# Performance work log

Hardware: AMD Instinct MI355X
Metric: run time of the kernel (lower is better)

## Reference

```python
import jax, jax.numpy as jnp
import numpy as np

HEAD_DIM = 64
NUM_HEADS = 16
ROPE_BASE = 10000.0


def _rope_cos_sin(seq_len, head_dim, dtype):
    inv_freq = 1.0 / (ROPE_BASE ** (jnp.arange(0, head_dim, 2, dtype=jnp.float32) / head_dim))
    t = jnp.arange(seq_len, dtype=jnp.float32)
    freqs = jnp.outer(t, inv_freq)                      # [S, D/2]
    emb = jnp.concatenate([freqs, freqs], axis=-1)      # [S, D]
    return jnp.cos(emb).astype(dtype), jnp.sin(emb).astype(dtype)


def _rotate_half(x):
    x1, x2 = jnp.split(x, 2, axis=-1)
    return jnp.concatenate([-x2, x1], axis=-1)


def setup_inputs() -> dict:
    key = jax.random.key(0)
    ks = jax.random.split(key, 5)
    B, S, H = 2, 2048, 1024
    x = jax.random.normal(ks[0], (B, S, H), dtype=jnp.float32)
    attention_mask = jnp.ones((B, S), dtype=jnp.float32)
    scale = 0.02
    Wq = jax.random.normal(ks[1], (H, H), dtype=jnp.float32) * scale
    Wk = jax.random.normal(ks[2], (H, H), dtype=jnp.float32) * scale
    Wv = jax.random.normal(ks[3], (H, H), dtype=jnp.float32) * scale
    Wo = jax.random.normal(ks[4], (H, H), dtype=jnp.float32) * scale
    return {"x": x, "attention_mask": attention_mask, "Wq": Wq, "Wk": Wk, "Wv": Wv, "Wo": Wo}


def reference(x, attention_mask, Wq, Wk, Wv, Wo):
    B, S, H = x.shape
    nh, hd = NUM_HEADS, HEAD_DIM
    scale = hd ** -0.5

    # nn.Linear semantics: y = x @ W^T  (W is [out, in])
    q = jnp.einsum('bsh,oh->bso', x, Wq).reshape(B, S, nh, hd).transpose(0, 2, 1, 3)
    k = jnp.einsum('bsh,oh->bso', x, Wk).reshape(B, S, nh, hd).transpose(0, 2, 1, 3)
    v = jnp.einsum('bsh,oh->bso', x, Wv).reshape(B, S, nh, hd).transpose(0, 2, 1, 3)

    cos, sin = _rope_cos_sin(S, hd, x.dtype)            # [S, hd]
    cos = cos[None, None, :, :]
    sin = sin[None, None, :, :]
    q = q * cos + _rotate_half(q) * sin
    k = k * cos + _rotate_half(k) * sin

    attn = jnp.einsum('bhqd,bhkd->bhqk', q, k) * scale  # [B, nh, S, S]
    mask = (1.0 - attention_mask.astype(x.dtype))[:, None, None, :] * jnp.finfo(x.dtype).min
    attn = attn + mask
    attn = jax.nn.softmax(attn, axis=-1)
    out = jnp.einsum('bhqk,bhkd->bhqd', attn, v)        # [B, nh, S, hd]
    out = out.transpose(0, 2, 1, 3).reshape(B, S, nh * hd)
    return jnp.einsum('bso,ho->bsh', out, Wo)
```

## Files before the change

### kernel.cpp

```cpp
#include <hip/hip_runtime.h>
#include <math.h>

#define BB 2
#define SS 2048
#define HH 1024
#define NH 16
#define HD 64
#define MM (BB*SS)

typedef __attribute__((ext_vector_type(8))) _Float16 f16x8;
typedef __attribute__((ext_vector_type(4))) float f32x4;

__device__ __forceinline__ unsigned short f2h(float f) {
    union { _Float16 h; unsigned short u; } c;
    c.h = (_Float16)f;
    return c.u;
}

__device__ __forceinline__ void gld16(const void* g, void* s) {
    __builtin_amdgcn_global_load_lds(
        (const __attribute__((address_space(1))) void*)g,
        (__attribute__((address_space(3))) void*)s, 16, 0, 0);
}

__global__ __launch_bounds__(256) void prep(
    const float* __restrict__ x,
    const float* __restrict__ Wq, const float* __restrict__ Wk,
    const float* __restrict__ Wv, const float* __restrict__ Wo,
    unsigned short* __restrict__ xf, unsigned short* __restrict__ wf,
    float* __restrict__ ctab, float* __restrict__ stab)
{
    int gtid = blockIdx.x * 256 + threadIdx.x;
    if (gtid < SS * 32) {
        int s = gtid >> 5, i = gtid & 31;
        double invf = pow(10000.0, -(double)i / 32.0);
        double a = (double)s * invf;
        ctab[gtid] = (float)cos(a);
        stab[gtid] = (float)sin(a);
    }
    for (int it = gtid; it < 2097152; it += 524288) {
        float4 v; unsigned short* d; size_t off;
        if (it < 1048576) {
            off = (size_t)it * 4;
            v = *(const float4*)(x + off);
            d = xf;
        } else {
            off = (size_t)(it - 1048576) * 4;
            int row = (int)(off >> 10);
            const float* W = row < 1024 ? Wq : row < 2048 ? Wk : row < 3072 ? Wv : Wo;
            v = *(const float4*)(W + (((size_t)(row & 1023)) << 10) + (off & 1023));
            d = wf;
        }
        *(ushort4*)(d + off) = make_ushort4(f2h(v.x), f2h(v.y), f2h(v.z), f2h(v.w));
    }
}

template<int MODE>
__global__ __launch_bounds__(256, 3) void gemm3(
    const unsigned short* __restrict__ Axf,
    const unsigned short* __restrict__ Wf,
    const float* __restrict__ ctab, const float* __restrict__ stab,
    unsigned short* __restrict__ qo, unsigned short* __restrict__ ko,
    unsigned short* __restrict__ vo, float* __restrict__ fout)
{
    __shared__ __align__(16) short lsA[2][128*32];
    __shared__ __align__(16) short lsB[2][128*32];

    const int t = threadIdx.x;
    const int m0 = blockIdx.x * 128;
    const int brow0 = (MODE == 0 ? 0 : 3072) + blockIdx.y * 128;
    const int lane = t & 63, wv = t >> 6;
    const int wm = (wv >> 1) * 64, wn = (wv & 1) * 64;
    const int fr = lane & 15, fg = lane >> 4;

    const int srow = t >> 2, pc = t & 3;
    const int scx = (pc ^ ((srow >> 1) & 3)) * 8;
    const int lo  = srow * 32 + pc * 8;
    const size_t gA0 = (size_t)(m0 + srow) * HH + scx;
    const size_t gA1 = (size_t)(m0 + 64 + srow) * HH + scx;
    const size_t gB0 = (size_t)(brow0 + srow) * HH + scx;
    const size_t gB1 = (size_t)(brow0 + 64 + srow) * HH + scx;

    f32x4 acc[4][4] = {};

#define STAGE(sel, kk) do { \
        gld16(Axf + gA0 + (kk), &lsA[sel][lo]);            \
        gld16(Wf  + gB0 + (kk), &lsB[sel][lo]);            \
        gld16(Axf + gA1 + (kk), &lsA[sel][lo + 64*32]);    \
        gld16(Wf  + gB1 + (kk), &lsB[sel][lo + 64*32]);    \
    } while (0)

    STAGE(0, 0);
    __syncthreads();

    int cur = 0;
    for (int k0 = 0; k0 < HH; k0 += 32) {
        if (k0 + 32 < HH) STAGE(cur ^ 1, k0 + 32);

        f16x8 ah[4], bh[4];
        const int swz = (fg ^ ((fr >> 1) & 3)) * 8;
        #pragma unroll
        for (int mi = 0; mi < 4; ++mi)
            ah[mi] = *(const f16x8*)&lsA[cur][(wm + 16*mi + fr)*32 + swz];
        #pragma unroll
        for (int ni = 0; ni < 4; ++ni)
            bh[ni] = *(const f16x8*)&lsB[cur][(wn + 16*ni + fr)*32 + swz];

        __builtin_amdgcn_s_setprio(1);
        #pragma unroll
        for (int mi = 0; mi < 4; ++mi)
            #pragma unroll
            for (int ni = 0; ni < 4; ++ni)
                acc[mi][ni] = __builtin_amdgcn_mfma_f32_16x16x32_f16(ah[mi], bh[ni], acc[mi][ni], 0, 0, 0);
        __builtin_amdgcn_s_setprio(0);
        __syncthreads();
        cur ^= 1;
    }
#undef STAGE

    if (MODE == 0) {
        const int mat = brow0 >> 10;
        const int obase = (brow0 & 1023) + wn;
        const int h = obase >> 6;
        #pragma unroll
        for (int mi = 0; mi < 4; ++mi)
            #pragma unroll
            for (int rr = 0; rr < 4; ++rr) {
                int m = m0 + wm + 16*mi + 4*fg + rr;
                int b = m >> 11, s = m & (SS - 1);
                float v[4];
                #pragma unroll
                for (int ni = 0; ni < 4; ++ni) v[ni] = acc[mi][ni][rr];
                if (mat < 2) {
                    #pragma unroll
                    for (int ni = 0; ni < 2; ++ni) {
                        int i = 16*ni + fr;
                        float c = ctab[s*32 + i], sn = stab[s*32 + i];
                        float v1 = v[ni], v2 = v[ni + 2];
                        v[ni]     = v1*c - v2*sn;
                        v[ni + 2] = v2*c + v1*sn;
                    }
                }
                size_t base = ((size_t)(b*NH + h) * SS + s) * HD;
                #pragma unroll
                for (int ni = 0; ni < 4; ++ni) {
                    int d = 16*ni + fr;
                    unsigned short hb = f2h(v[ni]);
                    if (mat == 0)      qo[base + d] = hb;
                    else if (mat == 1) ko[base + (d ^ ((s & 7) << 3))] = hb;
                    else {
                        size_t va = ((size_t)(b*NH + h) * HD + d) * SS
                                  + (s & ~63) + ((s & 63) ^ ((d & 7) << 3));
                        vo[va] = hb;
                    }
                }
            }
    } else {
        const int n0 = blockIdx.y * 128 + wn;
        #pragma unroll
        for (int mi = 0; mi < 4; ++mi)
            #pragma unroll
            for (int rr = 0; rr < 4; ++rr) {
                int m = m0 + wm + 16*mi + 4*fg + rr;
                #pragma unroll
                for (int ni = 0; ni < 4; ++ni)
                    fout[(size_t)m * HH + n0 + 16*ni + fr] = acc[mi][ni][rr];
            }
    }
}

__global__ __launch_bounds__(256, 4) void attn(
    const unsigned short* __restrict__ qg, const unsigned short* __restrict__ kg,
    const unsigned short* __restrict__ vtg, const float* __restrict__ mask,
    unsigned short* __restrict__ cf)
{
    __shared__ __align__(16) short Ks[2][64*64];
    __shared__ __align__(16) short Vs[2][64*64];
    __shared__ __align__(16) short Ps[64*64];

    const int t = threadIdx.x, lane = t & 63, wv = t >> 6;
    const int fr = lane & 15, fg = lane >> 4;
    const int bh = blockIdx.y, b = bh >> 4, h = bh & 15;
    const int q0 = blockIdx.x * 64;

    const unsigned short* kgb = kg  + (size_t)bh*SS*HD;
    const unsigned short* vgb = vtg + (size_t)bh*HD*SS;

    f16x8 qa[2];
    #pragma unroll
    for (int kc = 0; kc < 2; ++kc)
        qa[kc] = *(const f16x8*)&qg[((size_t)bh*SS + q0 + 16*wv + fr)*HD + kc*32 + fg*8];

    f32x4 o[4] = {};
    float lpart[4] = {0.f, 0.f, 0.f, 0.f};

    const int srow = t >> 3, sg = t & 7;

    gld16(kgb + (size_t)(srow)*HD + sg*8,      &Ks[0][srow*64 + sg*8]);
    gld16(kgb + (size_t)(32+srow)*HD + sg*8,   &Ks[0][(32+srow)*64 + sg*8]);
    gld16(vgb + (size_t)srow*SS + sg*8,        &Vs[0][srow*64 + sg*8]);
    gld16(vgb + (size_t)(32+srow)*SS + sg*8,   &Vs[0][(32+srow)*64 + sg*8]);
    __syncthreads();

    int cur = 0;
    for (int kt = 0; kt < SS/64; ++kt) {
        const int k0 = kt * 64;
        if (kt + 1 < SS/64) {
            const int kn = k0 + 64;
            gld16(kgb + (size_t)(kn+srow)*HD + sg*8,      &Ks[cur^1][srow*64 + sg*8]);
            gld16(kgb + (size_t)(kn+32+srow)*HD + sg*8,   &Ks[cur^1][(32+srow)*64 + sg*8]);
            gld16(vgb + (size_t)srow*SS + kn + sg*8,      &Vs[cur^1][srow*64 + sg*8]);
            gld16(vgb + (size_t)(32+srow)*SS + kn + sg*8, &Vs[cur^1][(32+srow)*64 + sg*8]);
        }

        f32x4 sc[4] = {};
        __builtin_amdgcn_s_setprio(1);
        #pragma unroll
        for (int kc = 0; kc < 2; ++kc) {
            f16x8 kb[4];
            #pragma unroll
            for (int nf = 0; nf < 4; ++nf) {
                int row = 16*nf + fr;
                int gr = (4*kc + fg) ^ (fr & 7);
                kb[nf] = *(const f16x8*)&Ks[cur][row*64 + gr*8];
            }
            #pragma unroll
            for (int nf = 0; nf < 4; ++nf)
                sc[nf] = __builtin_amdgcn_mfma_f32_16x16x32_f16(qa[kc], kb[nf], sc[nf], 0, 0, 0);
        }
        __builtin_amdgcn_s_setprio(0);

        float madd[4];
        #pragma unroll
        for (int nf = 0; nf < 4; ++nf)
            madd[nf] = (1.0f - mask[(size_t)b*SS + k0 + 16*nf + fr]) * (-1.0e38f);

        #pragma unroll
        for (int rr = 0; rr < 4; ++rr) {
            const int prow = 16*wv + 4*fg + rr;
            #pragma unroll
            for (int nf = 0; nf < 4; ++nf) {
                float p = __builtin_amdgcn_exp2f(fmaf(sc[nf][rr], 0.18033688f, madd[nf]));
                lpart[rr] += p;
                int col = 16*nf + fr;
                int gr = (col >> 3) ^ (prow & 7);
                Ps[prow*64 + gr*8 + (col & 7)] = (short)f2h(p);
            }
        }

        __builtin_amdgcn_s_setprio(1);
        #pragma unroll
        for (int kc = 0; kc < 2; ++kc) {
            int grk = (4*kc + fg) ^ (fr & 7);
            f16x8 pa = *(const f16x8*)&Ps[(16*wv + fr)*64 + grk*8];
            #pragma unroll
            for (int df = 0; df < 4; ++df) {
                f16x8 vb = *(const f16x8*)&Vs[cur][(16*df + fr)*64 + grk*8];
                o[df] = __builtin_amdgcn_mfma_f32_16x16x32_f16(pa, vb, o[df], 0, 0, 0);
            }
        }
        __builtin_amdgcn_s_setprio(0);
        __syncthreads();
        cur ^= 1;
    }

    #pragma unroll
    for (int rr = 0; rr < 4; ++rr) {
        float l = lpart[rr];
        #pragma unroll
        for (int d = 1; d < 16; d <<= 1) l += __shfl_xor(l, d);
        float inv = 1.0f / l;
        int srw = q0 + 16*wv + 4*fg + rr;
        size_t base = ((size_t)b*SS + srw)*HH + h*HD;
        #pragma unroll
        for (int df = 0; df < 4; ++df)
            cf[base + 16*df + fr] = f2h(o[df][rr] * inv);
    }
}

extern "C" void kernel_launch(void* const* d_in, const int* in_sizes, int n_in,
                              void* d_out, int out_size, void* d_ws, size_t ws_size,
                              hipStream_t stream) {
    const float* x    = (const float*)d_in[0];
    const float* mask = (const float*)d_in[1];
    const float* Wq   = (const float*)d_in[2];
    const float* Wk   = (const float*)d_in[3];
    const float* Wv   = (const float*)d_in[4];
    const float* Wo   = (const float*)d_in[5];
    float* out = (float*)d_out;

    const size_t T = (size_t)MM * HH;
    unsigned short* xf = (unsigned short*)d_ws;
    unsigned short* wf = xf + T;
    unsigned short* qt = wf + T;
    unsigned short* kt = qt + T;
    unsigned short* vt = kt + T;
    float* ctab = (float*)(vt + T);
    float* stab = ctab + SS*32;
    unsigned short* cf = xf;

    prep<<<2048, 256, 0, stream>>>(x, Wq, Wk, Wv, Wo, xf, wf, ctab, stab);
    gemm3<0><<<dim3(MM/128, 3*HH/128), 256, 0, stream>>>(xf, wf, ctab, stab,
                                                         qt, kt, vt, nullptr);
    attn<<<dim3(SS/64, BB*NH), 256, 0, stream>>>(qt, kt, vt, mask, cf);
    gemm3<1><<<dim3(MM/128, HH/128), 256, 0, stream>>>(cf, wf, nullptr, nullptr,
                                                       nullptr, nullptr, nullptr, out);
}
```

Baseline: 129.1 us.

## Enlarge attention tile to 128 queries, transpose MFMA operands, precompute mask and q scale

The attention kernel now runs 512 threads covering 128 query rows per block, so each K/V tile loaded into LDS serves twice as many queries and each thread issues only one load per tile. The MFMA operands are swapped so each lane holds four consecutive key scores for a single query row. That allows packed half-precision P stores, one running sum per lane, and packed vectorised output stores. The softmax scale is folded into Q in the projection GEMM, and the additive mask is precomputed once in prep and read as float4. Costs are fewer blocks (lower occupancy and less grid parallelism) and rounding of the pre-scaled Q to fp16.

```diff
diff --git a/kernel.cpp b/kernel.cpp
--- a/kernel.cpp
+++ b/kernel.cpp
@@ -9,7 +9,10 @@
 #define MM (BB*SS)
 
 typedef __attribute__((ext_vector_type(8))) _Float16 f16x8;
+typedef __attribute__((ext_vector_type(2))) __fp16 hf16x2;
 typedef __attribute__((ext_vector_type(4))) float f32x4;
+
+#define QSCALE 0.18033688011112042f
 
 __device__ __forceinline__ unsigned short f2h(float f) {
     union { _Float16 h; unsigned short u; } c;
@@ -17,6 +20,12 @@
     return c.u;
 }
 
+__device__ __forceinline__ unsigned int pkh(float a, float b) {
+    union { hf16x2 h; unsigned int u; } c;
+    c.h = __builtin_amdgcn_cvt_pkrtz(a, b);
+    return c.u;
+}
+
 __device__ __forceinline__ void gld16(const void* g, void* s) {
     __builtin_amdgcn_global_load_lds(
         (const __attribute__((address_space(1))) void*)g,
@@ -24,11 +33,11 @@
 }
 
 __global__ __launch_bounds__(256) void prep(
-    const float* __restrict__ x,
+    const float* __restrict__ x, const float* __restrict__ mask,
     const float* __restrict__ Wq, const float* __restrict__ Wk,
     const float* __restrict__ Wv, const float* __restrict__ Wo,
     unsigned short* __restrict__ xf, unsigned short* __restrict__ wf,
-    float* __restrict__ ctab, float* __restrict__ stab)
+    float* __restrict__ ctab, float* __restrict__ stab, float* __restrict__ mt)
 {
     int gtid = blockIdx.x * 256 + threadIdx.x;
     if (gtid < SS * 32) {
@@ -38,6 +47,8 @@
         ctab[gtid] = (float)cos(a);
         stab[gtid] = (float)sin(a);
     }
+    if (gtid < BB * SS)
+        mt[gtid] = (1.0f - mask[gtid]) * (-1.0e38f);
     for (int it = gtid; it < 2097152; it += 524288) {
         float4 v; unsigned short* d; size_t off;
         if (it < 1048576) {
@@ -140,6 +151,10 @@
                         v[ni]     = v1*c - v2*sn;
                         v[ni + 2] = v2*c + v1*sn;
                     }
+                }
+                if (mat == 0) {
+                    #pragma unroll
+                    for (int ni = 0; ni < 4; ++ni) v[ni] *= QSCALE;
                 }
                 size_t base = ((size_t)(b*NH + h) * SS + s) * HD;
                 #pragma unroll
@@ -169,22 +184,23 @@
     }
 }
 
-__global__ __launch_bounds__(256, 4) void attn(
+__global__ __launch_bounds__(512, 2) void attn(
     const unsigned short* __restrict__ qg, const unsigned short* __restrict__ kg,
-    const unsigned short* __restrict__ vtg, const float* __restrict__ mask,
+    const unsigned short* __restrict__ vtg, const float* __restrict__ mt,
     unsigned short* __restrict__ cf)
 {
     __shared__ __align__(16) short Ks[2][64*64];
     __shared__ __align__(16) short Vs[2][64*64];
-    __shared__ __align__(16) short Ps[64*64];
+    __shared__ __align__(16) short Ps[128*64];
 
     const int t = threadIdx.x, lane = t & 63, wv = t >> 6;
-    const int fr = lane & 15, fg = lane >> 4;
+    const int fr = lane & 15, fg = lane >> 4, frx = fr & 7;
     const int bh = blockIdx.y, b = bh >> 4, h = bh & 15;
-    const int q0 = blockIdx.x * 64;
+    const int q0 = blockIdx.x * 128;
 
     const unsigned short* kgb = kg  + (size_t)bh*SS*HD;
     const unsigned short* vgb = vtg + (size_t)bh*HD*SS;
+    const float* mtb = mt + (size_t)b*SS;
 
     f16x8 qa[2];
     #pragma unroll
@@ -192,14 +208,13 @@
         qa[kc] = *(const f16x8*)&qg[((size_t)bh*SS + q0 + 16*wv + fr)*HD + kc*32 + fg*8];
 
     f32x4 o[4] = {};
-    float lpart[4] = {0.f, 0.f, 0.f, 0.f};
+    float lpart = 0.f;
+    const int pbase = (wv*16 + fr) * 64;
 
     const int srow = t >> 3, sg = t & 7;
 
-    gld16(kgb + (size_t)(srow)*HD + sg*8,      &Ks[0][srow*64 + sg*8]);
-    gld16(kgb + (size_t)(32+srow)*HD + sg*8,   &Ks[0][(32+srow)*64 + sg*8]);
-    gld16(vgb + (size_t)srow*SS + sg*8,        &Vs[0][srow*64 + sg*8]);
-    gld16(vgb + (size_t)(32+srow)*SS + sg*8,   &Vs[0][(32+srow)*64 + sg*8]);
+    gld16(kgb + (size_t)srow*HD + sg*8, &Ks[0][srow*64 + sg*8]);
+    gld16(vgb + (size_t)srow*SS + sg*8, &Vs[0][srow*64 + sg*8]);
     __syncthreads();
 
     int cur = 0;
@@ -207,56 +222,48 @@
         const int k0 = kt * 64;
         if (kt + 1 < SS/64) {
             const int kn = k0 + 64;
-            gld16(kgb + (size_t)(kn+srow)*HD + sg*8,      &Ks[cur^1][srow*64 + sg*8]);
-            gld16(kgb + (size_t)(kn+32+srow)*HD + sg*8,   &Ks[cur^1][(32+srow)*64 + sg*8]);
-            gld16(vgb + (size_t)srow*SS + kn + sg*8,      &Vs[cur^1][srow*64 + sg*8]);
-            gld16(vgb + (size_t)(32+srow)*SS + kn + sg*8, &Vs[cur^1][(32+srow)*64 + sg*8]);
-        }
+            gld16(kgb + (size_t)(kn+srow)*HD + sg*8, &Ks[cur^1][srow*64 + sg*8]);
+            gld16(vgb + (size_t)srow*SS + kn + sg*8, &Vs[cur^1][srow*64 + sg*8]);
+        }
+
+        float4 m4[4];
+        #pragma unroll
+        for (int nf = 0; nf < 4; ++nf)
+            m4[nf] = *(const float4*)&mtb[k0 + 16*nf + 4*fg];
 
         f32x4 sc[4] = {};
         __builtin_amdgcn_s_setprio(1);
         #pragma unroll
         for (int kc = 0; kc < 2; ++kc) {
-            f16x8 kb[4];
             #pragma unroll
             for (int nf = 0; nf < 4; ++nf) {
-                int row = 16*nf + fr;
-                int gr = (4*kc + fg) ^ (fr & 7);
-                kb[nf] = *(const f16x8*)&Ks[cur][row*64 + gr*8];
+                int gr = (4*kc + fg) ^ frx;
+                f16x8 kb = *(const f16x8*)&Ks[cur][(16*nf + fr)*64 + gr*8];
+                sc[nf] = __builtin_amdgcn_mfma_f32_16x16x32_f16(kb, qa[kc], sc[nf], 0, 0, 0);
             }
-            #pragma unroll
-            for (int nf = 0; nf < 4; ++nf)
-                sc[nf] = __builtin_amdgcn_mfma_f32_16x16x32_f16(qa[kc], kb[nf], sc[nf], 0, 0, 0);
         }
         __builtin_amdgcn_s_setprio(0);
 
-        float madd[4];
-        #pragma unroll
-        for (int nf = 0; nf < 4; ++nf)
-            madd[nf] = (1.0f - mask[(size_t)b*SS + k0 + 16*nf + fr]) * (-1.0e38f);
-
-        #pragma unroll
-        for (int rr = 0; rr < 4; ++rr) {
-            const int prow = 16*wv + 4*fg + rr;
-            #pragma unroll
-            for (int nf = 0; nf < 4; ++nf) {
-                float p = __builtin_amdgcn_exp2f(fmaf(sc[nf][rr], 0.18033688f, madd[nf]));
-                lpart[rr] += p;
-                int col = 16*nf + fr;
-                int gr = (col >> 3) ^ (prow & 7);
-                Ps[prow*64 + gr*8 + (col & 7)] = (short)f2h(p);
-            }
+        #pragma unroll
+        for (int nf = 0; nf < 4; ++nf) {
+            float p0 = __builtin_amdgcn_exp2f(sc[nf][0] + m4[nf].x);
+            float p1 = __builtin_amdgcn_exp2f(sc[nf][1] + m4[nf].y);
+            float p2 = __builtin_amdgcn_exp2f(sc[nf][2] + m4[nf].z);
+            float p3 = __builtin_amdgcn_exp2f(sc[nf][3] + m4[nf].w);
+            lpart += (p0 + p1) + (p2 + p3);
+            uint2 w; w.x = pkh(p0, p1); w.y = pkh(p2, p3);
+            *(uint2*)&Ps[pbase + (((2*nf + (fg >> 1)) ^ frx) * 8) + 4*(fg & 1)] = w;
         }
 
         __builtin_amdgcn_s_setprio(1);
         #pragma unroll
         for (int kc = 0; kc < 2; ++kc) {
-            int grk = (4*kc + fg) ^ (fr & 7);
-            f16x8 pa = *(const f16x8*)&Ps[(16*wv + fr)*64 + grk*8];
+            int gr = (4*kc + fg) ^ frx;
+            f16x8 pa = *(const f16x8*)&Ps[pbase + gr*8];
             #pragma unroll
             for (int df = 0; df < 4; ++df) {
-                f16x8 vb = *(const f16x8*)&Vs[cur][(16*df + fr)*64 + grk*8];
-                o[df] = __builtin_amdgcn_mfma_f32_16x16x32_f16(pa, vb, o[df], 0, 0, 0);
+                f16x8 vb = *(const f16x8*)&Vs[cur][(16*df + fr)*64 + gr*8];
+                o[df] = __builtin_amdgcn_mfma_f32_16x16x32_f16(vb, pa, o[df], 0, 0, 0);
             }
         }
         __builtin_amdgcn_s_setprio(0);
@@ -264,17 +271,17 @@
         cur ^= 1;
     }
 
+    float l = lpart;
+    l += __shfl_xor(l, 16);
+    l += __shfl_xor(l, 32);
+    float inv = 1.0f / l;
+    size_t base = ((size_t)b*SS + q0 + 16*wv + fr)*HH + h*HD;
     #pragma unroll
-    for (int rr = 0; rr < 4; ++rr) {
-        float l = lpart[rr];
-        #pragma unroll
-        for (int d = 1; d < 16; d <<= 1) l += __shfl_xor(l, d);
-        float inv = 1.0f / l;
-        int srw = q0 + 16*wv + 4*fg + rr;
-        size_t base = ((size_t)b*SS + srw)*HH + h*HD;
-        #pragma unroll
-        for (int df = 0; df < 4; ++df)
-            cf[base + 16*df + fr] = f2h(o[df][rr] * inv);
+    for (int df = 0; df < 4; ++df) {
+        uint2 w;
+        w.x = pkh(o[df][0]*inv, o[df][1]*inv);
+        w.y = pkh(o[df][2]*inv, o[df][3]*inv);
+        *(uint2*)&cf[base + 16*df + 4*fg] = w;
     }
 }
 
@@ -297,12 +304,13 @@
     unsigned short* vt = kt + T;
     float* ctab = (float*)(vt + T);
     float* stab = ctab + SS*32;
+    float* mt   = stab + SS*32;
     unsigned short* cf = xf;
 
-    prep<<<2048, 256, 0, stream>>>(x, Wq, Wk, Wv, Wo, xf, wf, ctab, stab);
+    prep<<<2048, 256, 0, stream>>>(x, mask, Wq, Wk, Wv, Wo, xf, wf, ctab, stab, mt);
     gemm3<0><<<dim3(MM/128, 3*HH/128), 256, 0, stream>>>(xf, wf, ctab, stab,
                                                          qt, kt, vt, nullptr);
-    attn<<<dim3(SS/64, BB*NH), 256, 0, stream>>>(qt, kt, vt, mask, cf);
+    attn<<<dim3(SS/128, BB*NH), 512, 0, stream>>>(qt, kt, vt, mt, cf);
     gemm3<1><<<dim3(MM/128, HH/128), 256, 0, stream>>>(cf, wf, nullptr, nullptr,
                                                        nullptr, nullptr, nullptr, out);
 }
```

Result: faster. 121.6 us (-5.8%).
